# Optimization experiments

Hardware: AMD Instinct MI355X
Metric: run time of the kernel (lower is better)

Reference implementation:

```python
import jax, jax.numpy as jnp
import numpy as np

N, D_IN, D_OUT = 8192, 64, 64
MAX_NEIGH = 100  # module keeps only the last 100 nonzero neighbors per row
DECAY = 0.5


def setup_inputs() -> dict:
    key = jax.random.key(0)
    k1, k2, k3, k4 = jax.random.split(key, 4)
    stdv = 1.0 / np.sqrt(D_OUT)
    inputs = {
        "input": jax.random.normal(k1, (N, D_IN), dtype=jnp.float32),
        "adj": jax.random.randint(k2, (N, N), 0, 2).astype(jnp.float32),
        "weight": jax.random.uniform(k3, (D_IN, D_OUT), minval=-stdv, maxval=stdv, dtype=jnp.float32),
        "bias": jax.random.uniform(k4, (D_OUT,), minval=-stdv, maxval=stdv, dtype=jnp.float32),
    }
    return inputs


def reference(input, adj, weight, bias):
    # support[n, f] = (input @ weight)[n, f]
    support = input @ weight  # [N, d_out]

    # The torch module, per row a: idx = sorted nonzero cols, keep last 100,
    # then decay(k-1, support[idx]) = sum_j 0.5**(k-1-j) * support[idx[j]].
    # Vectorized: rank each nonzero by cumsum along the row, keep ranks in the
    # last-100 window, and weight by DECAY**(k - position_within_window).
    mask = (adj != 0).astype(support.dtype)            # [N, N]
    rank = jnp.cumsum(mask, axis=1)                    # 1-based rank at nonzeros
    deg = rank[:, -1:]                                 # [N, 1] row degree
    k = jnp.minimum(deg, float(MAX_NEIGH))             # neighbors actually used
    pos = rank - (deg - k)                             # 1..k inside the window
    w = mask * jnp.where(pos > 0, DECAY ** (k - pos), 0.0)  # [N, N] decay weights

    out = w @ support + bias                           # rows with deg==0 stay zero pre-bias... 
    # NOTE: torch returns zeros(out_features)+bias for empty rows too, matching w@support=0 + bias.
    return out
```

## Files before the change

### kernel.cpp

```cpp
#include <hip/hip_runtime.h>

#define N 8192
#define D 64
#define MAXN 100

__global__ __launch_bounds__(256) void support_kernel(
    const float* __restrict__ input,
    const float* __restrict__ weight,
    float* __restrict__ support) {
  __shared__ float w[D * D];
  __shared__ float inr[4 * D];

  int tid = threadIdx.x;
  const float4* w4 = (const float4*)weight;
  float4* sw4 = (float4*)w;
  for (int i = tid; i < (D * D) / 4; i += 256) sw4[i] = w4[i];
  inr[tid] = input[(size_t)blockIdx.x * 256 + tid];
  __syncthreads();

  int rloc = tid >> 6;
  int d    = tid & 63;

  float acc = 0.f;
#pragma unroll
  for (int k = 0; k < D; ++k) {
    acc += inr[rloc * D + k] * w[k * D + d];
  }
  support[(size_t)blockIdx.x * 256 + tid] = acc;
}

__global__ __launch_bounds__(256) void gather_kernel(
    const float* __restrict__ adj,
    const float* __restrict__ support,
    const float* __restrict__ bias,
    float* __restrict__ out) {
  __shared__ int idxbuf[4][MAXN];

  int tid  = threadIdx.x;
  int lane = tid & 63;
  int wv   = tid >> 6;
  int row  = blockIdx.x * 4 + wv;

  const float* arow = adj + (size_t)row * N;

  int found = 0;
  for (int base = N - 256; base >= 0 && found < MAXN; base -= 256) {
    const float4 v = *(const float4*)(arow + base + lane * 4);
    bool nz0 = (v.x != 0.0f), nz1 = (v.y != 0.0f);
    bool nz2 = (v.z != 0.0f), nz3 = (v.w != 0.0f);
    unsigned long long m0 = __ballot(nz0), m1 = __ballot(nz1);
    unsigned long long m2 = __ballot(nz2), m3 = __ballot(nz3);
    unsigned long long hi = ~((2ull << lane) - 1ull);
    int aboveL = __popcll(m0 & hi) + __popcll(m1 & hi) +
                 __popcll(m2 & hi) + __popcll(m3 & hi);
    int b1 = (int)((m1 >> lane) & 1ull);
    int b2 = (int)((m2 >> lane) & 1ull);
    int b3 = (int)((m3 >> lane) & 1ull);
    int t3 = found + aboveL;
    int t2 = t3 + b3;
    int t1 = t2 + b2;
    int t0 = t1 + b1;
    int col = base + lane * 4;
    if (nz3 && t3 < MAXN) idxbuf[wv][t3] = col + 3;
    if (nz2 && t2 < MAXN) idxbuf[wv][t2] = col + 2;
    if (nz1 && t1 < MAXN) idxbuf[wv][t1] = col + 1;
    if (nz0 && t0 < MAXN) idxbuf[wv][t0] = col + 0;
    found += __popcll(m0) + __popcll(m1) + __popcll(m2) + __popcll(m3);
    if (found > MAXN) found = MAXN;
  }

  __syncthreads();

  int g  = lane >> 4;
  int sl = lane & 15;

  float ax = 0.f, ay = 0.f, az = 0.f, aw = 0.f;
#pragma unroll 4
  for (int tb = 0; tb < found; tb += 4) {
    int t = tb + g;
    bool ok = (t < found);
    int j = ok ? idxbuf[wv][t] : 0;
    float wgt = ok ? ldexpf(1.0f, -t) : 0.0f;
    const float4 s4 = *(const float4*)(support + (size_t)j * D + sl * 4);
    ax += wgt * s4.x;
    ay += wgt * s4.y;
    az += wgt * s4.z;
    aw += wgt * s4.w;
  }

  ax += __shfl_xor(ax, 16); ay += __shfl_xor(ay, 16);
  az += __shfl_xor(az, 16); aw += __shfl_xor(aw, 16);
  ax += __shfl_xor(ax, 32); ay += __shfl_xor(ay, 32);
  az += __shfl_xor(az, 32); aw += __shfl_xor(aw, 32);

  if (lane < 16) {
    const float4 b4 = *(const float4*)(bias + sl * 4);
    float4 o;
    o.x = ax + b4.x; o.y = ay + b4.y; o.z = az + b4.z; o.w = aw + b4.w;
    *(float4*)(out + (size_t)row * D + sl * 4) = o;
  }
}

extern "C" void kernel_launch(void* const* d_in, const int* in_sizes, int n_in,
                              void* d_out, int out_size, void* d_ws, size_t ws_size,
                              hipStream_t stream) {
  const float* input  = (const float*)d_in[0];
  const float* adj    = (const float*)d_in[1];
  const float* weight = (const float*)d_in[2];
  const float* bias   = (const float*)d_in[3];
  float* out = (float*)d_out;

  float* support = (float*)d_ws;

  support_kernel<<<N / 4, 256, 0, stream>>>(input, weight, support);
  gather_kernel<<<N / 4, 256, 0, stream>>>(adj, support, bias, out);
}
```

Measured before the change: 313.4 us.

## Reassociate GCN product to gather raw inputs then apply weight in fused kernel

Replaces the separate support = input@weight kernel with a single fused kernel that gathers decay-weighted input rows and then multiplies the aggregated 64-vector by the weight matrix held in shared memory. This removes one kernel launch and the global write/read of the support intermediate. In exchange each block reloads the full weight into LDS and performs a per-row 64x64 matvec, increasing shared memory use and possibly lowering occupancy.

```diff
diff --git a/kernel.cpp b/kernel.cpp
--- a/kernel.cpp
+++ b/kernel.cpp
@@ -4,42 +4,26 @@
 #define D 64
 #define MAXN 100
 
-__global__ __launch_bounds__(256) void support_kernel(
+__global__ __launch_bounds__(256) void gcn_fused_kernel(
     const float* __restrict__ input,
+    const float* __restrict__ adj,
     const float* __restrict__ weight,
-    float* __restrict__ support) {
-  __shared__ float w[D * D];
-  __shared__ float inr[4 * D];
-
-  int tid = threadIdx.x;
-  const float4* w4 = (const float4*)weight;
-  float4* sw4 = (float4*)w;
-  for (int i = tid; i < (D * D) / 4; i += 256) sw4[i] = w4[i];
-  inr[tid] = input[(size_t)blockIdx.x * 256 + tid];
-  __syncthreads();
-
-  int rloc = tid >> 6;
-  int d    = tid & 63;
-
-  float acc = 0.f;
-#pragma unroll
-  for (int k = 0; k < D; ++k) {
-    acc += inr[rloc * D + k] * w[k * D + d];
-  }
-  support[(size_t)blockIdx.x * 256 + tid] = acc;
-}
-
-__global__ __launch_bounds__(256) void gather_kernel(
-    const float* __restrict__ adj,
-    const float* __restrict__ support,
     const float* __restrict__ bias,
     float* __restrict__ out) {
+  __shared__ float wsh[D * D];
   __shared__ int idxbuf[4][MAXN];
+  __shared__ float accbuf[4][D];
 
   int tid  = threadIdx.x;
   int lane = tid & 63;
   int wv   = tid >> 6;
   int row  = blockIdx.x * 4 + wv;
+
+  {
+    const float4* w4 = (const float4*)weight;
+    float4* sw4 = (float4*)wsh;
+    for (int i = tid; i < (D * D) / 4; i += 256) sw4[i] = w4[i];
+  }
 
   const float* arow = adj + (size_t)row * N;
 
@@ -81,7 +65,7 @@
     bool ok = (t < found);
     int j = ok ? idxbuf[wv][t] : 0;
     float wgt = ok ? ldexpf(1.0f, -t) : 0.0f;
-    const float4 s4 = *(const float4*)(support + (size_t)j * D + sl * 4);
+    const float4 s4 = *(const float4*)(input + (size_t)j * D + sl * 4);
     ax += wgt * s4.x;
     ay += wgt * s4.y;
     az += wgt * s4.z;
@@ -94,11 +78,17 @@
   az += __shfl_xor(az, 32); aw += __shfl_xor(aw, 32);
 
   if (lane < 16) {
-    const float4 b4 = *(const float4*)(bias + sl * 4);
-    float4 o;
-    o.x = ax + b4.x; o.y = ay + b4.y; o.z = az + b4.z; o.w = aw + b4.w;
-    *(float4*)(out + (size_t)row * D + sl * 4) = o;
+    float4* ab4 = (float4*)accbuf[wv];
+    float4 a4; a4.x = ax; a4.y = ay; a4.z = az; a4.w = aw;
+    ab4[sl] = a4;
   }
+
+  float acc = bias[lane];
+#pragma unroll
+  for (int k = 0; k < D; ++k) {
+    acc += accbuf[wv][k] * wsh[k * D + lane];
+  }
+  out[(size_t)row * D + lane] = acc;
 }
 
 extern "C" void kernel_launch(void* const* d_in, const int* in_sizes, int n_in,
@@ -110,8 +100,5 @@
   const float* bias   = (const float*)d_in[3];
   float* out = (float*)d_out;
 
-  float* support = (float*)d_ws;
-
-  support_kernel<<<N / 4, 256, 0, stream>>>(input, weight, support);
-  gather_kernel<<<N / 4, 256, 0, stream>>>(adj, support, bias, out);
+  gcn_fused_kernel<<<N / 4, 256, 0, stream>>>(input, adj, weight, bias, out);
 }
```

New measurement: 310.1 us. About the same (-1.0%).
